# Kernel optimization log

Measured on AMD Instinct MI355X. Metric: run time of the kernel, lower is better.

## Reference

```python
import jax, jax.numpy as jnp
import numpy as np

DE_NEIGHBORS = 3
DEPTH = 2


def square_distance(src, dst):
    # src: [B, N, 3], dst: [B, S, 3] -> pairwise squared L2 [B, N, S]
    return (jnp.sum(src * src, axis=-1)[:, :, None]
            + jnp.sum(dst * dst, axis=-1)[:, None, :]
            - 2.0 * jnp.einsum('bnc,bsc->bns', src, dst))


def propagate(xyz1, xyz2, points1, points2):
    # xyz1: [B, N, 3] fine coords; xyz2: [B, S, 3] coarse coords
    # points1: [B, C1, N] skip feats; points2: [B, C2, S] coarse feats
    pts2 = points2.transpose(0, 2, 1)  # [B, S, C2]
    dists = square_distance(xyz1, xyz2)  # [B, N, S]
    neg_d, idx = jax.lax.top_k(-dists, DE_NEIGHBORS)  # smallest-k distances
    d = -neg_d  # [B, N, K]
    w = 1.0 / (d + 1e-8)
    w = w / jnp.sum(w, axis=-1, keepdims=True)  # [B, N, K]
    # gather neighbor features: [B, N, K, C2]
    gathered = jax.vmap(lambda p, i: p[i])(pts2, idx)
    interp = jnp.sum(gathered * w[..., None], axis=2)  # [B, N, C2]
    m = interp.mean()
    s = jnp.std(interp - m, ddof=1)  # torch.std default is unbiased
    interp = (interp - m) / (s + 1e-5)
    new_points = jnp.concatenate([points1.transpose(0, 2, 1), interp], axis=-1)
    return new_points.transpose(0, 2, 1)  # [B, C1+C2, N]


def setup_inputs() -> dict:
    key = jax.random.key(0)
    ks = jax.random.split(key, 6)
    B = 8
    return {
        'xyz0': jax.random.normal(ks[0], (B, 8192, 3), jnp.float32),
        'xyz1': jax.random.normal(ks[1], (B, 2048, 3), jnp.float32),
        'xyz2': jax.random.normal(ks[2], (B, 512, 3), jnp.float32),
        'x0': jax.random.normal(ks[3], (B, 128, 8192), jnp.float32),
        'x1': jax.random.normal(ks[4], (B, 256, 2048), jnp.float32),
        'x2': jax.random.normal(ks[5], (B, 512, 512), jnp.float32),
    }


def reference(xyz0, xyz1, xyz2, x0, x1, x2):
    # forward reverses the lists: index 0 = coarsest level
    xyz_list = [xyz2, xyz1, xyz0]
    x_list = [x2, x1, x0]
    x = x_list[0]
    for i in range(DEPTH):
        x = propagate(xyz_list[i + 1], xyz_list[i], x_list[i + 1], x)
    return x  # [8, 128+256+512, 8192]
```

## Files before the change

### kernel.cpp

```cpp
#include <hip/hip_runtime.h>
#include <cstdint>
#include <math.h>


__device__ __forceinline__ void dev_merge6(const float* __restrict__ cd,
                                           const int* __restrict__ ci,
                                           int& o0, int& o1, int& o2,
                                           float& w0, float& w1, float& w2) {
    float d0 = 1e30f, d1 = 1e30f, d2 = 1e30f;
    int j0 = 0, j1 = 0, j2 = 0;
#pragma unroll
    for (int k = 0; k < 6; ++k) {
        const float d = cd[k];
        const int s = ci[k];
        const bool lt0 = d < d0, lt1 = d < d1, lt2 = d < d2;
        d2 = lt1 ? d1 : (lt2 ? d : d2);
        j2 = lt1 ? j1 : (lt2 ? s : j2);
        d1 = lt0 ? d0 : (lt1 ? d : d1);
        j1 = lt0 ? j0 : (lt1 ? s : j1);
        d0 = lt0 ? d : d0;
        j0 = lt0 ? s : j0;
    }
    const float a = 1.0f / (d0 + 1e-8f);
    const float b = 1.0f / (d1 + 1e-8f);
    const float c = 1.0f / (d2 + 1e-8f);
    const float ws = (a + b) + c;
    o0 = j0; o1 = j1; o2 = j2;
    w0 = a / ws; w1 = b / ws; w2 = c / ws;
}

template <int CHUNK>
__device__ __forceinline__ void dev_knn_lds(const float* __restrict__ fine,
                                            const float* __restrict__ coarse,
                                            int N, int S, int nch,
                                            int b, int nb, int chunk, int tid,
                                            float4* __restrict__ lc,
                                            float* __restrict__ cand_d,
                                            int* __restrict__ cand_i) {
#pragma clang fp contract(off)
    const int s0 = chunk * CHUNK;
    const float* cb = coarse + ((size_t)b * S + s0) * 3;
    for (int s = tid; s < CHUNK; s += 256) {
        const float x = cb[3 * s], y = cb[3 * s + 1], z = cb[3 * s + 2];
        lc[s] = make_float4(x, y, z, (x * x + y * y) + z * z);
    }
    __syncthreads();
    const int n = nb * 256 + tid;
    const float* fp = fine + ((size_t)b * N + n) * 3;
    const float px = fp[0], py = fp[1], pz = fp[2];
    const float psq = (px * px + py * py) + pz * pz;
    float d0 = 1e30f, d1 = 1e30f, d2 = 1e30f;
    int i0 = 0, i1 = 0, i2 = 0;
#pragma unroll 4
    for (int s = 0; s < CHUNK; ++s) {
        const float4 c = lc[s];
        const float dot = (px * c.x + py * c.y) + pz * c.z;
        const float d = fmaf(-2.0f, dot, psq + c.w);
        if (__any(d < d2)) {
            const bool lt0 = d < d0, lt1 = d < d1, lt2 = d < d2;
            d2 = lt1 ? d1 : (lt2 ? d : d2);
            i2 = lt1 ? i1 : (lt2 ? s : i2);
            d1 = lt0 ? d0 : (lt1 ? d : d1);
            i1 = lt0 ? i0 : (lt1 ? s : i1);
            d0 = lt0 ? d : d0;
            i0 = lt0 ? s : i0;
        }
    }
    const size_t p = (((size_t)b * N + n) * nch + chunk) * 3;
    cand_d[p] = d0; cand_d[p + 1] = d1; cand_d[p + 2] = d2;
    cand_i[p] = s0 + i0; cand_i[p + 1] = s0 + i1; cand_i[p + 2] = s0 + i2;
}

__device__ __forceinline__ void dev_transpose(const float* __restrict__ in,
                                              float* __restrict__ out,
                                              int C, long in_bs, long out_bs, int out_rs,
                                              int b, int rt, int ct, int tid,
                                              float* __restrict__ tile ) {
    const int r0 = rt * 32, c0 = ct * 32;
    const float* inb = in + (size_t)b * in_bs;
    float* outb = out + (size_t)b * out_bs;
    const int tx = tid & 31, ty = tid >> 5;
#pragma unroll
    for (int i = 0; i < 32; i += 8) {
        tile[(ty + i) * 33 + tx] = inb[(size_t)(r0 + ty + i) * C + (c0 + tx)];
    }
    __syncthreads();
#pragma unroll
    for (int i = 0; i < 32; i += 8) {
        outb[(size_t)(c0 + ty + i) * out_rs + (r0 + tx)] = tile[tx * 33 + (ty + i)];
    }
}

__global__ __launch_bounds__(256) void k_front(const float* __restrict__ xyz0,
                                               const float* __restrict__ xyz1,
                                               const float* __restrict__ xyz2,
                                               const float* __restrict__ x0,
                                               const float* __restrict__ x1,
                                               const float* __restrict__ x2,
                                               float* __restrict__ pts1,
                                               float* __restrict__ inter,
                                               float* __restrict__ out,
                                               float* __restrict__ cand_d2,
                                               int* __restrict__ cand_i2,
                                               float* __restrict__ cand_d1,
                                               int* __restrict__ cand_i1) {
    __shared__ __align__(16) char smem[16384];
    const int id = blockIdx.x;
    const int tid = threadIdx.x;
    if (id < 512) {
        dev_knn_lds<1024>(xyz0, xyz1, 8192, 2048, 2,
                          id >> 6, id & 31, (id >> 5) & 1, tid,
                          (float4*)smem, cand_d2, cand_i2);
    } else if (id < 640) {
        const int t = id - 512;
        dev_knn_lds<256>(xyz1, xyz2, 2048, 512, 2,
                         t >> 4, t & 7, (t >> 3) & 1, tid,
                         (float4*)smem, cand_d1, cand_i1);
    } else if (id < 8832) {
        const size_t i = (size_t)(id - 640) * 256 + tid;
        const size_t b = i >> 18;
        const size_t off = i & (((size_t)1 << 18) - 1);
        const float4* src = (const float4*)(x0 + b * (size_t)128 * 8192);
        float4* dst = (float4*)(out + b * (size_t)896 * 8192);
        dst[off] = src[off];
    } else if (id < 12928) {
        const int t = id - 8832;
        const int ct = t & 63, rt = (t >> 6) & 7, b = t >> 9;
        dev_transpose(x1, inter, 2048, 256 * 2048, (long)2048 * 768, 768,
                      b, rt, ct, tid, (float*)smem);
    } else {
        const int t = id - 12928;
        const int ct = t & 15, rt = (t >> 4) & 15, b = t >> 8;
        dev_transpose(x2, pts1, 512, 512 * 512, 512 * 512, 512,
                      b, rt, ct, tid, (float*)smem);
    }
}

__global__ __launch_bounds__(256) void k_interp_stats(const float* __restrict__ pts,
                                                      const float* __restrict__ cand_d,
                                                      const int* __restrict__ cand_i,
                                                      int N, int S, int C,
                                                      double* __restrict__ partials) {
    __shared__ int   si[32][3];
    __shared__ float sw[32][3];
    const int b = blockIdx.x, nb = blockIdx.y, cb = blockIdx.z;
    const int n0 = nb * 32;
    const int tid = threadIdx.x;
    if (tid < 32) {
        const size_t pt = (size_t)b * N + n0 + tid;
        dev_merge6(cand_d + pt * 6, cand_i + pt * 6,
                   si[tid][0], si[tid][1], si[tid][2],
                   sw[tid][0], sw[tid][1], sw[tid][2]);
    }
    __syncthreads();
    const int C4 = C >> 2;
    const float4* pbf = (const float4*)(pts + (size_t)b * S * C) + (cb * 64);
    const int f = tid & 63;
    const int pg = tid >> 6;
    double ls = 0.0, lq = 0.0;
#pragma unroll
    for (int g = 0; g < 8; ++g) {
        const int nl = g * 4 + pg;
        const size_t r0 = (size_t)si[nl][0] * C4;
        const size_t r1 = (size_t)si[nl][1] * C4;
        const size_t r2 = (size_t)si[nl][2] * C4;
        const float w0 = sw[nl][0], w1 = sw[nl][1], w2 = sw[nl][2];
        const float4 a = pbf[r0 + f], c = pbf[r1 + f], e = pbf[r2 + f];
        const float vx = (w0 * a.x + w1 * c.x) + w2 * e.x;
        const float vy = (w0 * a.y + w1 * c.y) + w2 * e.y;
        const float vz = (w0 * a.z + w1 * c.z) + w2 * e.z;
        const float vw = (w0 * a.w + w1 * c.w) + w2 * e.w;
        ls += (double)vx + (double)vy + (double)vz + (double)vw;
        lq += (double)vx * vx + (double)vy * vy + (double)vz * vz + (double)vw * vw;
    }
    __shared__ double sa[256], sb[256];
    sa[tid] = ls; sb[tid] = lq; __syncthreads();
    for (int s = 128; s > 0; s >>= 1) {
        if (tid < s) { sa[tid] += sa[tid + s]; sb[tid] += sb[tid + s]; }
        __syncthreads();
    }
    if (tid == 0) {
        const size_t pl = ((size_t)cb * gridDim.x + b) * gridDim.y + nb;
        partials[2 * pl] = sa[0]; partials[2 * pl + 1] = sb[0];
    }
}

__global__ __launch_bounds__(1024) void k_finalize(const double* __restrict__ partials,
                                                   int P, double nelem,
                                                   float* __restrict__ stats) {
    __shared__ double sa[1024], sb[1024];
    double ls = 0.0, lq = 0.0;
    for (int i = threadIdx.x; i < P; i += 1024) { ls += partials[2 * i]; lq += partials[2 * i + 1]; }
    const int t = threadIdx.x;
    sa[t] = ls; sb[t] = lq; __syncthreads();
    for (int s = 512; s > 0; s >>= 1) {
        if (t < s) { sa[t] += sa[t + s]; sb[t] += sb[t + s]; }
        __syncthreads();
    }
    if (t == 0) {
        const double sum = sa[0], sq = sb[0];
        const double m = sum / nelem;
        const double var = (sq - sum * sum / nelem) / (nelem - 1.0);
        const double sd = sqrt(var > 0.0 ? var : 0.0);
        stats[0] = (float)m;
        stats[1] = (float)(1.0 / (sd + 1e-5));
    }
}

__global__ __launch_bounds__(256) void k_interp1_write(const float* __restrict__ pts,
                                                       const float* __restrict__ cand_d,
                                                       const int* __restrict__ cand_i,
                                                       const float* __restrict__ stats,
                                                       float* __restrict__ inter) {
    const float m = stats[0], rs = stats[1];
    const int b = blockIdx.x;
    const int n0 = blockIdx.y * 4;
    const int tid = threadIdx.x;
    const int pt = tid >> 6, f = tid & 63;
    const size_t p = (size_t)b * 2048 + n0 + pt;
    int i0, i1, i2; float w0, w1, w2;
    dev_merge6(cand_d + p * 6, cand_i + p * 6, i0, i1, i2, w0, w1, w2);
    const float4* pb4 = (const float4*)(pts + (size_t)b * 512 * 512);
    const size_t r0 = (size_t)i0 * 128, r1 = (size_t)i1 * 128, r2 = (size_t)i2 * 128;
    float4* out4 = (float4*)(inter + p * 768 + 256);
#pragma unroll
    for (int k = 0; k < 2; ++k) {
        const int c = f + k * 64;
        const float4 a = pb4[r0 + c], d = pb4[r1 + c], e = pb4[r2 + c];
        float4 v;
        v.x = (((w0 * a.x + w1 * d.x) + w2 * e.x) - m) * rs;
        v.y = (((w0 * a.y + w1 * d.y) + w2 * e.y) - m) * rs;
        v.z = (((w0 * a.z + w1 * d.z) + w2 * e.z) - m) * rs;
        v.w = (((w0 * a.w + w1 * d.w) + w2 * e.w) - m) * rs;
        out4[c] = v;
    }
}

__global__ __launch_bounds__(256) void k_interp2_write(const float* __restrict__ pts,
                                                       const float* __restrict__ cand_d,
                                                       const int* __restrict__ cand_i,
                                                       const float* __restrict__ stats,
                                                       float* __restrict__ out) {
    __shared__ float tile[64][65];
    __shared__ int   si[64][3];
    __shared__ float sw[64][3];
    const float m = stats[0], rs = stats[1];
    const int b = blockIdx.x, nt = blockIdx.y, cc = blockIdx.z;
    const int n0 = nt * 64, c0 = cc * 64;
    const int tid = threadIdx.x;
    if (tid < 64) {
        const size_t pt = (size_t)b * 8192 + n0 + tid;
        dev_merge6(cand_d + pt * 6, cand_i + pt * 6,
                   si[tid][0], si[tid][1], si[tid][2],
                   sw[tid][0], sw[tid][1], sw[tid][2]);
    }
    __syncthreads();
    const float* pb = pts + (size_t)b * 2048 * 768 + c0;
    const int cl = tid & 63;
    const int pg = tid >> 6;
#pragma unroll
    for (int pass = 0; pass < 16; ++pass) {
        const int nl = pass * 4 + pg;
        const float v = (sw[nl][0] * pb[(size_t)si[nl][0] * 768 + cl]
                       + sw[nl][1] * pb[(size_t)si[nl][1] * 768 + cl])
                       + sw[nl][2] * pb[(size_t)si[nl][2] * 768 + cl];
        tile[nl][cl] = (v - m) * rs;
    }
    __syncthreads();
    float* ob = out + (size_t)b * 896 * 8192 + (size_t)(128 + c0) * 8192 + n0;
    const int tn = tid & 63, tc0 = tid >> 6;
#pragma unroll
    for (int pass = 0; pass < 16; ++pass) {
        const int tc = pass * 4 + tc0;
        ob[(size_t)tc * 8192 + tn] = tile[tn][tc];
    }
}

extern "C" void kernel_launch(void* const* d_in, const int* in_sizes, int n_in,
                              void* d_out, int out_size, void* d_ws, size_t ws_size,
                              hipStream_t stream) {
    const float* xyz0 = (const float*)d_in[0];
    const float* xyz1 = (const float*)d_in[1];
    const float* xyz2 = (const float*)d_in[2];
    const float* x0   = (const float*)d_in[3];
    const float* x1   = (const float*)d_in[4];
    const float* x2   = (const float*)d_in[5];
    float* out = (float*)d_out;
    char* ws = (char*)d_ws;

    size_t off = 0;
    auto alloc = [&](size_t bytes) {
        size_t o = off;
        off = (off + bytes + 255) & ~(size_t)255;
        return o;
    };
    float*  stats    = (float*)(ws + alloc(8 * sizeof(float)));
    double* partials = (double*)(ws + alloc((size_t)6144 * 2 * sizeof(double)));
    float*  pts1     = (float*)(ws + alloc((size_t)8 * 512 * 512 * 4));
    float*  inter    = (float*)(ws + alloc((size_t)8 * 2048 * 768 * 4));
    float*  cand_d2  = (float*)(ws + alloc((size_t)65536 * 6 * 4));
    int*    cand_i2  = (int*)(ws + alloc((size_t)65536 * 6 * 4));
    float*  cand_d1  = (float*)(ws + alloc((size_t)16384 * 6 * 4));
    int*    cand_i1  = (int*)(ws + alloc((size_t)16384 * 6 * 4));

    k_front<<<14976, 256, 0, stream>>>(xyz0, xyz1, xyz2, x0, x1, x2,
                                       pts1, inter, out,
                                       cand_d2, cand_i2, cand_d1, cand_i1);
    k_interp_stats<<<dim3(8, 64, 2), 256, 0, stream>>>(
        pts1, cand_d1, cand_i1, 2048, 512, 512, partials);
    k_finalize<<<1, 1024, 0, stream>>>(partials, 1024, (double)8 * 2048 * 512, stats);
    k_interp1_write<<<dim3(8, 512), 256, 0, stream>>>(pts1, cand_d1, cand_i1, stats, inter);
    k_interp_stats<<<dim3(8, 256, 3), 256, 0, stream>>>(
        inter, cand_d2, cand_i2, 8192, 2048, 768, partials);
    k_finalize<<<1, 1024, 0, stream>>>(partials, 6144, (double)8 * 8192 * 768, stats + 2);
    k_interp2_write<<<dim3(8, 128, 12), 256, 0, stream>>>(inter, cand_d2, cand_i2,
                                                          stats + 2, out);
}
```

Baseline: 192.6 us.

## Defer level-1 normalization by folding its affine into level-2 stats

Level-1 interpolation now writes unnormalized values and computes its sum and sum-of-squares partials in the same kernel. This removes the separate stats pass and the first finalize launch. Because level-2 interpolation is linear, the level-1 affine normalization is folded into the level-2 statistics. A single combined finalize produces per-channel-range alpha/beta coefficients, which the last kernel applies. The cost is extra algebra in double precision and slightly different float rounding, because normalization is applied once after interpolation rather than before.

Measured after the change: 187.8 us. 1.03x faster.

```diff
diff --git a/kernel.cpp b/kernel.cpp
--- a/kernel.cpp
+++ b/kernel.cpp
@@ -136,6 +136,62 @@
     }
 }
 
+__global__ __launch_bounds__(256) void k_interp1_fused(const float* __restrict__ pts,
+                                                       const float* __restrict__ cand_d,
+                                                       const int* __restrict__ cand_i,
+                                                       float* __restrict__ inter,
+                                                       double* __restrict__ partials1) {
+    __shared__ int   si[16][3];
+    __shared__ float sw[16][3];
+    const int b = blockIdx.x, nb = blockIdx.y;
+    const int n0 = nb * 16;
+    const int tid = threadIdx.x;
+    if (tid < 16) {
+        const size_t pt = (size_t)b * 2048 + n0 + tid;
+        dev_merge6(cand_d + pt * 6, cand_i + pt * 6,
+                   si[tid][0], si[tid][1], si[tid][2],
+                   sw[tid][0], sw[tid][1], sw[tid][2]);
+    }
+    __syncthreads();
+    const float4* pb4 = (const float4*)(pts + (size_t)b * 512 * 512);
+    const int pg = tid >> 6, f = tid & 63;
+    double ls = 0.0, lq = 0.0;
+#pragma unroll
+    for (int g = 0; g < 4; ++g) {
+        const int pl = g * 4 + pg;
+        const size_t p = (size_t)b * 2048 + n0 + pl;
+        const size_t r0 = (size_t)si[pl][0] * 128;
+        const size_t r1 = (size_t)si[pl][1] * 128;
+        const size_t r2 = (size_t)si[pl][2] * 128;
+        const float w0 = sw[pl][0], w1 = sw[pl][1], w2 = sw[pl][2];
+        float4* out4 = (float4*)(inter + p * 768 + 256);
+#pragma unroll
+        for (int k = 0; k < 2; ++k) {
+            const int c = f + k * 64;
+            const float4 a = pb4[r0 + c], d = pb4[r1 + c], e = pb4[r2 + c];
+            float4 v;
+            v.x = (w0 * a.x + w1 * d.x) + w2 * e.x;
+            v.y = (w0 * a.y + w1 * d.y) + w2 * e.y;
+            v.z = (w0 * a.z + w1 * d.z) + w2 * e.z;
+            v.w = (w0 * a.w + w1 * d.w) + w2 * e.w;
+            out4[c] = v;
+            ls += (double)v.x + (double)v.y + (double)v.z + (double)v.w;
+            lq += (double)v.x * v.x + (double)v.y * v.y
+                + (double)v.z * v.z + (double)v.w * v.w;
+        }
+    }
+    __shared__ double sa[256], sb[256];
+    sa[tid] = ls; sb[tid] = lq; __syncthreads();
+    for (int s = 128; s > 0; s >>= 1) {
+        if (tid < s) { sa[tid] += sa[tid + s]; sb[tid] += sb[tid + s]; }
+        __syncthreads();
+    }
+    if (tid == 0) {
+        const size_t pl = (size_t)b * gridDim.y + nb;
+        partials1[2 * pl] = sa[0]; partials1[2 * pl + 1] = sb[0];
+    }
+}
+
 __global__ __launch_bounds__(256) void k_interp_stats(const float* __restrict__ pts,
                                                       const float* __restrict__ cand_d,
                                                       const int* __restrict__ cand_i,
@@ -185,67 +241,67 @@
     }
 }
 
-__global__ __launch_bounds__(1024) void k_finalize(const double* __restrict__ partials,
-                                                   int P, double nelem,
-                                                   float* __restrict__ stats) {
-    __shared__ double sa[1024], sb[1024];
-    double ls = 0.0, lq = 0.0;
-    for (int i = threadIdx.x; i < P; i += 1024) { ls += partials[2 * i]; lq += partials[2 * i + 1]; }
+__global__ __launch_bounds__(256) void k_fin_combined(const double* __restrict__ partials1,
+                                                      int P1,
+                                                      const double* __restrict__ partials2,
+                                                      int P2, int P2lo,
+                                                      float* __restrict__ stats4) {
+    __shared__ double red[6][256];
     const int t = threadIdx.x;
-    sa[t] = ls; sb[t] = lq; __syncthreads();
-    for (int s = 512; s > 0; s >>= 1) {
-        if (t < s) { sa[t] += sa[t + s]; sb[t] += sb[t + s]; }
+    double s1 = 0.0, q1 = 0.0, s2l = 0.0, q2l = 0.0, s2h = 0.0, q2h = 0.0;
+    for (int i = t; i < P1; i += 256) { s1 += partials1[2 * i]; q1 += partials1[2 * i + 1]; }
+    for (int i = t; i < P2; i += 256) {
+        const double s = partials2[2 * i], q = partials2[2 * i + 1];
+        if (i < P2lo) { s2l += s; q2l += q; } else { s2h += s; q2h += q; }
+    }
+    red[0][t] = s1; red[1][t] = q1; red[2][t] = s2l;
+    red[3][t] = q2l; red[4][t] = s2h; red[5][t] = q2h;
+    __syncthreads();
+    for (int s = 128; s > 0; s >>= 1) {
+        if (t < s) {
+#pragma unroll
+            for (int r = 0; r < 6; ++r) red[r][t] += red[r][t + s];
+        }
         __syncthreads();
     }
     if (t == 0) {
-        const double sum = sa[0], sq = sb[0];
-        const double m = sum / nelem;
-        const double var = (sq - sum * sum / nelem) / (nelem - 1.0);
-        const double sd = sqrt(var > 0.0 ? var : 0.0);
-        stats[0] = (float)m;
-        stats[1] = (float)(1.0 / (sd + 1e-5));
-    }
-}
-
-__global__ __launch_bounds__(256) void k_interp1_write(const float* __restrict__ pts,
-                                                       const float* __restrict__ cand_d,
-                                                       const int* __restrict__ cand_i,
-                                                       const float* __restrict__ stats,
-                                                       float* __restrict__ inter) {
-    const float m = stats[0], rs = stats[1];
-    const int b = blockIdx.x;
-    const int n0 = blockIdx.y * 4;
-    const int tid = threadIdx.x;
-    const int pt = tid >> 6, f = tid & 63;
-    const size_t p = (size_t)b * 2048 + n0 + pt;
-    int i0, i1, i2; float w0, w1, w2;
-    dev_merge6(cand_d + p * 6, cand_i + p * 6, i0, i1, i2, w0, w1, w2);
-    const float4* pb4 = (const float4*)(pts + (size_t)b * 512 * 512);
-    const size_t r0 = (size_t)i0 * 128, r1 = (size_t)i1 * 128, r2 = (size_t)i2 * 128;
-    float4* out4 = (float4*)(inter + p * 768 + 256);
-#pragma unroll
-    for (int k = 0; k < 2; ++k) {
-        const int c = f + k * 64;
-        const float4 a = pb4[r0 + c], d = pb4[r1 + c], e = pb4[r2 + c];
-        float4 v;
-        v.x = (((w0 * a.x + w1 * d.x) + w2 * e.x) - m) * rs;
-        v.y = (((w0 * a.y + w1 * d.y) + w2 * e.y) - m) * rs;
-        v.z = (((w0 * a.z + w1 * d.z) + w2 * e.z) - m) * rs;
-        v.w = (((w0 * a.w + w1 * d.w) + w2 * e.w) - m) * rs;
-        out4[c] = v;
+        const double nelem1 = 8388608.0;
+        const double cnt2   = 50331648.0;
+        const double cnthi  = 33554432.0;
+        const double S1 = red[0][0], Q1 = red[1][0];
+        const double m1 = S1 / nelem1;
+        const double v1 = (Q1 - S1 * S1 / nelem1) / (nelem1 - 1.0);
+        const double sd1 = sqrt(v1 > 0.0 ? v1 : 0.0);
+        const float rs1f = (float)(1.0 / (sd1 + 1e-5));
+        const float m1f = (float)m1;
+        const double a1 = (double)rs1f;
+        const double b1 = -(double)m1f * (double)rs1f;
+        const double S2l = red[2][0], Q2l = red[3][0];
+        const double S2h = red[4][0], Q2h = red[5][0];
+        const double Sf = S2l + a1 * S2h + b1 * cnthi;
+        const double Qf = Q2l + a1 * a1 * Q2h + 2.0 * a1 * b1 * S2h + b1 * b1 * cnthi;
+        const double m2 = Sf / cnt2;
+        const double v2 = (Qf - Sf * Sf / cnt2) / (cnt2 - 1.0);
+        const double sd2 = sqrt(v2 > 0.0 ? v2 : 0.0);
+        const double rs2 = 1.0 / (sd2 + 1e-5);
+        stats4[0] = (float)rs2;
+        stats4[1] = (float)(-m2 * rs2);
+        stats4[2] = (float)(a1 * rs2);
+        stats4[3] = (float)((b1 - m2) * rs2);
     }
 }
 
 __global__ __launch_bounds__(256) void k_interp2_write(const float* __restrict__ pts,
                                                        const float* __restrict__ cand_d,
                                                        const int* __restrict__ cand_i,
-                                                       const float* __restrict__ stats,
+                                                       const float* __restrict__ stats4,
                                                        float* __restrict__ out) {
     __shared__ float tile[64][65];
     __shared__ int   si[64][3];
     __shared__ float sw[64][3];
-    const float m = stats[0], rs = stats[1];
     const int b = blockIdx.x, nt = blockIdx.y, cc = blockIdx.z;
+    const float alpha = (cc < 4) ? stats4[0] : stats4[2];
+    const float beta  = (cc < 4) ? stats4[1] : stats4[3];
     const int n0 = nt * 64, c0 = cc * 64;
     const int tid = threadIdx.x;
     if (tid < 64) {
@@ -264,7 +320,7 @@
         const float v = (sw[nl][0] * pb[(size_t)si[nl][0] * 768 + cl]
                        + sw[nl][1] * pb[(size_t)si[nl][1] * 768 + cl])
                        + sw[nl][2] * pb[(size_t)si[nl][2] * 768 + cl];
-        tile[nl][cl] = (v - m) * rs;
+        tile[nl][cl] = alpha * v + beta;
     }
     __syncthreads();
     float* ob = out + (size_t)b * 896 * 8192 + (size_t)(128 + c0) * 8192 + n0;
@@ -294,25 +350,24 @@
         off = (off + bytes + 255) & ~(size_t)255;
         return o;
     };
-    float*  stats    = (float*)(ws + alloc(8 * sizeof(float)));
-    double* partials = (double*)(ws + alloc((size_t)6144 * 2 * sizeof(double)));
-    float*  pts1     = (float*)(ws + alloc((size_t)8 * 512 * 512 * 4));
-    float*  inter    = (float*)(ws + alloc((size_t)8 * 2048 * 768 * 4));
-    float*  cand_d2  = (float*)(ws + alloc((size_t)65536 * 6 * 4));
-    int*    cand_i2  = (int*)(ws + alloc((size_t)65536 * 6 * 4));
-    float*  cand_d1  = (float*)(ws + alloc((size_t)16384 * 6 * 4));
-    int*    cand_i1  = (int*)(ws + alloc((size_t)16384 * 6 * 4));
+    float*  stats4    = (float*)(ws + alloc(4 * sizeof(float)));
+    double* partials1 = (double*)(ws + alloc((size_t)1024 * 2 * sizeof(double)));
+    double* partials2 = (double*)(ws + alloc((size_t)6144 * 2 * sizeof(double)));
+    float*  pts1      = (float*)(ws + alloc((size_t)8 * 512 * 512 * 4));
+    float*  inter     = (float*)(ws + alloc((size_t)8 * 2048 * 768 * 4));
+    float*  cand_d2   = (float*)(ws + alloc((size_t)65536 * 6 * 4));
+    int*    cand_i2   = (int*)(ws + alloc((size_t)65536 * 6 * 4));
+    float*  cand_d1   = (float*)(ws + alloc((size_t)16384 * 6 * 4));
+    int*    cand_i1   = (int*)(ws + alloc((size_t)16384 * 6 * 4));
 
     k_front<<<14976, 256, 0, stream>>>(xyz0, xyz1, xyz2, x0, x1, x2,
                                        pts1, inter, out,
                                        cand_d2, cand_i2, cand_d1, cand_i1);
-    k_interp_stats<<<dim3(8, 64, 2), 256, 0, stream>>>(
-        pts1, cand_d1, cand_i1, 2048, 512, 512, partials);
-    k_finalize<<<1, 1024, 0, stream>>>(partials, 1024, (double)8 * 2048 * 512, stats);
-    k_interp1_write<<<dim3(8, 512), 256, 0, stream>>>(pts1, cand_d1, cand_i1, stats, inter);
+    k_interp1_fused<<<dim3(8, 128), 256, 0, stream>>>(
+        pts1, cand_d1, cand_i1, inter, partials1);
     k_interp_stats<<<dim3(8, 256, 3), 256, 0, stream>>>(
-        inter, cand_d2, cand_i2, 8192, 2048, 768, partials);
-    k_finalize<<<1, 1024, 0, stream>>>(partials, 6144, (double)8 * 8192 * 768, stats + 2);
+        inter, cand_d2, cand_i2, 8192, 2048, 768, partials2);
+    k_fin_combined<<<1, 256, 0, stream>>>(partials1, 1024, partials2, 6144, 2048, stats4);
     k_interp2_write<<<dim3(8, 128, 12), 256, 0, stream>>>(inter, cand_d2, cand_i2,
-                                                          stats + 2, out);
-}
+                                                          stats4, out);
+}
```
